# Optimization experiments

Hardware: AMD Instinct MI355X
Metric: run time of the kernel (lower is better)

The kernel has to match this reference:

```python
import jax, jax.numpy as jnp
import numpy as np

N, H, F = 131072, 256, 4096
MIN_FRAG = 3
LN_EPS = 1e-5
NORM_EPS = 1e-12
CONSISTENCY_FACTOR = 0.03
INTERMOLECULAR_WEIGHT = 0.2
SCALING_FACTOR = 0.05  # initial_strength at epoch 0 (progressive schedule, eval mode)


def _normalize(x):
    # torch F.normalize(p=2, dim=1): x / max(||x||, eps)
    n = jnp.linalg.norm(x, axis=-1, keepdims=True)
    return x / jnp.maximum(n, NORM_EPS)


def _frag_consistency(feat, frag_ids, valid):
    # size-weighted sum of per-fragment mean deviations == mean deviation over valid atoms
    m = valid.astype(feat.dtype)[:, None]
    seg_sum = jax.ops.segment_sum(feat * m, frag_ids, num_segments=F)
    seg_cnt = jax.ops.segment_sum(m, frag_ids, num_segments=F)
    means = seg_sum / jnp.maximum(seg_cnt, 1.0)  # scatter-mean over valid atoms
    sim = jnp.sum(_normalize(feat) * _normalize(means)[frag_ids], axis=-1)  # [N]
    dev = (1.0 - sim) * valid.astype(feat.dtype)
    return jnp.sum(dev) / jnp.maximum(jnp.sum(valid.astype(feat.dtype)), 1.0)


def setup_inputs() -> dict:
    key = jax.random.key(0)
    ks = jax.random.split(key, 8)
    return {
        "scalar_short": jax.random.normal(ks[0], (N, H), jnp.float32),
        "scalar_long": jax.random.normal(ks[1], (N, H), jnp.float32),
        "vector_short": jax.random.normal(ks[2], (N, 3, H), jnp.float32),
        "vector_long": jax.random.normal(ks[3], (N, 3, H), jnp.float32),
        "fragment_ids": jax.random.randint(ks[4], (N,), 0, F, dtype=jnp.int32),
        "ln_gamma": jnp.ones((H,), jnp.float32),
        "ln_beta": jnp.zeros((H,), jnp.float32),
        "W1": jax.random.normal(ks[5], (H, H), jnp.float32) / np.sqrt(H),
        "b1": jnp.zeros((H,), jnp.float32),
        "Wv": jax.random.normal(ks[6], (H, H), jnp.float32) / np.sqrt(H),
    }


def reference(scalar_short, scalar_long, vector_short, vector_long, fragment_ids,
              ln_gamma, ln_beta, W1, b1, Wv):
    # valid_mask: atoms belonging to fragments of size >= MIN_FRAG
    sizes = jax.ops.segment_sum(jnp.ones((N,), jnp.float32), fragment_ids, num_segments=F)
    valid = sizes[fragment_ids] >= MIN_FRAG  # [N] bool

    # scalar_projector: LayerNorm -> Linear -> SiLU (dropout identity at eval)
    mu = jnp.mean(scalar_short, axis=-1, keepdims=True)
    var = jnp.var(scalar_short, axis=-1, keepdims=True)
    xh = (scalar_short - mu) / jnp.sqrt(var + LN_EPS) * ln_gamma + ln_beta
    scalar_features = jax.nn.silu(xh @ W1.T + b1)  # [N, H]

    intra = _frag_consistency(scalar_features, fragment_ids, valid)

    # vector branch: per-atom magnitude = mean over 3 spatial comps of ||.||_2 over hidden
    vec_mag = jnp.mean(jnp.linalg.norm(vector_short, axis=2), axis=1, keepdims=True)  # [N,1]
    # Linear(bias=False) on mag.expand(-1,H) then [:, :1] == silu(mag * sum(Wv[0,:]))
    w0 = jnp.sum(Wv[0])
    vector_features = jax.nn.silu(vec_mag * w0)  # [N,1]
    vec_loss = _frag_consistency(vector_features, fragment_ids, valid)

    # interfragment differentiation over ALL atoms (no valid mask)
    cnt = jax.ops.segment_sum(jnp.ones((N, 1), jnp.float32), fragment_ids, num_segments=F)
    sfrag = jax.ops.segment_sum(scalar_features, fragment_ids, num_segments=F) / jnp.maximum(cnt, 1.0)
    vfrag = jax.ops.segment_sum(vec_mag, fragment_ids, num_segments=F) / jnp.maximum(cnt, 1.0)
    combined = _normalize(jnp.concatenate([sfrag, vfrag], axis=1))  # [F, H+1]
    sim = combined @ combined.T  # [F, F]
    off_sum = jnp.sum(sim) - jnp.trace(sim)
    inter = off_sum / (F * F - F + 1e-6)

    total = intra + vec_loss + INTERMOLECULAR_WEIGHT * inter
    return CONSISTENCY_FACTOR * total * SCALING_FACTOR
```

## Files before the change

kernel.cpp:

```cpp
#include <hip/hip_runtime.h>
#include <hip/hip_bf16.h>
#include <stdint.h>

#define NA 131072
#define HD 256
#define NF 4096
#define MINFRAG 3
#define LN_EPS 1e-5f
#define NEPS 1e-12f

#define OFF_CNT    0ull
#define OFF_VSUM   16384ull
#define OFF_VFSUM  32768ull
#define OFF_NVSUM  49152ull
#define OFF_FILL   65536ull
#define OFF_DBL    81920ull
#define OFF_SSUM   86016ull
#define OFF_NSUM   4280320ull
#define ZERO_BYTES 8474624ull
#define OFF_OFFS   8474624ull
#define OFF_SVEC   8491008ull
#define OFF_C0     8492032ull
#define OFF_W0     8493056ull
#define OFF_GBF    8493568ull
#define OFF_ORDER  8624640ull

#define IDX_TRACE 257
#define IDX_DEVS  258
#define IDX_DEVV  259
#define IDX_VCNT  260

typedef __attribute__((ext_vector_type(8))) short short8;
typedef __attribute__((ext_vector_type(4))) float f32x4;
union F4S8 { float4 f; short8 s; };
union BFU { __hip_bfloat16 b; unsigned short u; };

__device__ __forceinline__ unsigned short f2b(float x) {
    BFU t; t.b = __float2bfloat16(x); return t.u;
}
__device__ __forceinline__ float b2f(unsigned short u) {
    return __uint_as_float(((uint32_t)u) << 16);
}
__device__ __forceinline__ float silu_f(float x) { return x / (1.f + expf(-x)); }

__global__ __launch_bounds__(256) void k_prep(
    const float* __restrict__ W1, const float* __restrict__ gamma,
    const float* __restrict__ beta, const float* __restrict__ b1,
    const float* __restrict__ Wv,
    unsigned short* __restrict__ Gbf, float* __restrict__ svec,
    float* __restrict__ c0, float* __restrict__ w0) {
    __shared__ float red[8];
    int o = blockIdx.x;
    int t = threadIdx.x;
    if (o < HD) {
        float w = W1[(size_t)o * HD + t];
        unsigned short gb = f2b(w * gamma[t]);
        Gbf[(size_t)o * HD + t] = gb;
        float sp = b2f(gb);
        float cp = w * beta[t];
#pragma unroll
        for (int m = 32; m; m >>= 1) { sp += __shfl_xor(sp, m, 64); cp += __shfl_xor(cp, m, 64); }
        int wv = t >> 6;
        if ((t & 63) == 0) { red[wv] = sp; red[4 + wv] = cp; }
        __syncthreads();
        if (t == 0) {
            svec[o] = red[0] + red[1] + red[2] + red[3];
            c0[o]   = red[4] + red[5] + red[6] + red[7] + b1[o];
        }
    } else {
        float v = Wv[t];
#pragma unroll
        for (int m = 32; m; m >>= 1) v += __shfl_xor(v, m, 64);
        int wv = t >> 6;
        if ((t & 63) == 0) red[wv] = v;
        __syncthreads();
        if (t == 0) w0[0] = red[0] + red[1] + red[2] + red[3];
    }
}

__global__ __launch_bounds__(256) void k_stats(
    const float* __restrict__ vs, const int* __restrict__ fid,
    const float* __restrict__ w0p,
    int* __restrict__ cnt, float* __restrict__ vsum,
    float* __restrict__ vfsum, float* __restrict__ nvsum) {
    int gwave = (blockIdx.x * blockDim.x + threadIdx.x) >> 6;
    int lane = threadIdx.x & 63;
    int nw = (gridDim.x * blockDim.x) >> 6;
    float w0 = w0p[0];
    for (int i = gwave; i < NA; i += nw) {
        const float* base = vs + (size_t)i * 3 * HD;
        float4 v0 = ((const float4*)(base))[lane];
        float4 v1 = ((const float4*)(base + HD))[lane];
        float4 v2 = ((const float4*)(base + 2 * HD))[lane];
        float q0 = v0.x * v0.x + v0.y * v0.y + v0.z * v0.z + v0.w * v0.w;
        float q1 = v1.x * v1.x + v1.y * v1.y + v1.z * v1.z + v1.w * v1.w;
        float q2 = v2.x * v2.x + v2.y * v2.y + v2.z * v2.z + v2.w * v2.w;
#pragma unroll
        for (int m = 32; m; m >>= 1) {
            q0 += __shfl_xor(q0, m, 64);
            q1 += __shfl_xor(q1, m, 64);
            q2 += __shfl_xor(q2, m, 64);
        }
        if (lane == 0) {
            float vm = (sqrtf(q0) + sqrtf(q1) + sqrtf(q2)) * (1.f / 3.f);
            float vf = silu_f(vm * w0);
            float nv = vf / fmaxf(fabsf(vf), NEPS);
            int f = fid[i];
            atomicAdd(&cnt[f], 1);
            atomicAdd(&vsum[f], vm);
            atomicAdd(&vfsum[f], vf);
            atomicAdd(&nvsum[f], nv);
        }
    }
}

__global__ __launch_bounds__(256) void k_scan(const int* __restrict__ cnt,
                                              int* __restrict__ offs) {
    __shared__ int wsum[4];
    int t = threadIdx.x;
    int base = t * 16;
    int c[16];
    int tot = 0;
#pragma unroll
    for (int j = 0; j < 16; ++j) { c[j] = cnt[base + j]; tot += c[j]; }
    int lane = t & 63, w = t >> 6;
    int v = tot;
#pragma unroll
    for (int d = 1; d < 64; d <<= 1) {
        int o = __shfl_up(v, d, 64);
        if (lane >= d) v += o;
    }
    if (lane == 63) wsum[w] = v;
    __syncthreads();
    int wbase = 0;
    for (int i = 0; i < w; ++i) wbase += wsum[i];
    int run = wbase + v - tot;
#pragma unroll
    for (int j = 0; j < 16; ++j) { offs[base + j] = run; run += c[j]; }
}

__global__ __launch_bounds__(256) void k_scatter(
    const int* __restrict__ fid, const int* __restrict__ offs,
    int* __restrict__ fill, int* __restrict__ order) {
    int i = blockIdx.x * blockDim.x + threadIdx.x;
    if (i < NA) {
        int f = fid[i];
        int p = atomicAdd(&fill[f], 1);
        order[offs[f] + p] = i;
    }
}

__global__ __launch_bounds__(256) void k_gemm(
    const float* __restrict__ A, const unsigned short* __restrict__ Gbf,
    const float* __restrict__ svec, const float* __restrict__ c0,
    const int* __restrict__ order, const int* __restrict__ fid,
    const int* __restrict__ offs, const int* __restrict__ cnt,
    float* __restrict__ ssum, float* __restrict__ nsum) {
    __shared__ float4 As16[64 * 8];
    __shared__ float4 Bs16[256 * 8];
    __shared__ float muS[64], rsS[64], rnS[64];
    __shared__ float sqL[64][4];
    __shared__ int fragS[64];

    int tid = threadIdx.x;
    int lane = tid & 63, wid = tid >> 6;
    int r0 = blockIdx.x * 64;
    int rowT = tid >> 4;
    int c4 = tid & 15;

    if (tid < 64) {
        int gi = order[r0 + tid];
        muS[tid] = __int_as_float(gi);
        fragS[tid] = fid[gi];
    }
    __syncthreads();
    int rid[4];
#pragma unroll
    for (int p = 0; p < 4; ++p) rid[p] = __float_as_int(muS[16 * p + rowT]);
    __syncthreads();

    f32x4 acc[4][4] = {};
    float s1p[4] = {0, 0, 0, 0}, s2p[4] = {0, 0, 0, 0};

    for (int k0 = 0; k0 < HD; k0 += 64) {
#pragma unroll
        for (int p = 0; p < 4; ++p) {
            int row = 16 * p + rowT;
            float4 v = *(const float4*)(A + (size_t)rid[p] * HD + k0 + c4 * 4);
            s1p[p] += v.x + v.y + v.z + v.w;
            s2p[p] += v.x * v.x + v.y * v.y + v.z * v.z + v.w * v.w;
            ushort4 pk;
            pk.x = f2b(v.x); pk.y = f2b(v.y); pk.z = f2b(v.z); pk.w = f2b(v.w);
            int slot = row * 8 + ((c4 >> 1) ^ (row & 7));
            ((ushort4*)&As16[slot])[c4 & 1] = pk;
        }
#pragma unroll
        for (int p = 0; p < 8; ++p) {
            int u = p * 256 + tid;
            int n = u >> 3, cc = u & 7;
            float4 g = *(const float4*)(Gbf + (size_t)n * HD + k0 + cc * 8);
            Bs16[n * 8 + (cc ^ (n & 7))] = g;
        }
        __syncthreads();
#pragma unroll
        for (int kk = 0; kk < 2; ++kk) {
            int uo = kk * 4 + (lane >> 4);
            short8 a[4], b[4];
#pragma unroll
            for (int mi = 0; mi < 4; ++mi) {
                int r = mi * 16 + (lane & 15);
                F4S8 t_; t_.f = As16[r * 8 + (uo ^ (r & 7))];
                a[mi] = t_.s;
            }
#pragma unroll
            for (int ni = 0; ni < 4; ++ni) {
                int n = wid * 64 + ni * 16 + (lane & 15);
                F4S8 t_; t_.f = Bs16[n * 8 + (uo ^ (n & 7))];
                b[ni] = t_.s;
            }
#pragma unroll
            for (int mi = 0; mi < 4; ++mi)
#pragma unroll
                for (int ni = 0; ni < 4; ++ni)
                    acc[mi][ni] = __builtin_amdgcn_mfma_f32_16x16x32_bf16(
                        a[mi], b[ni], acc[mi][ni], 0, 0, 0);
        }
        __syncthreads();
    }
#pragma unroll
    for (int p = 0; p < 4; ++p) {
        float s1 = s1p[p], s2 = s2p[p];
#pragma unroll
        for (int m = 1; m < 16; m <<= 1) {
            s1 += __shfl_xor(s1, m, 64);
            s2 += __shfl_xor(s2, m, 64);
        }
        if (c4 == 0) {
            int row = 16 * p + rowT;
            float mu_ = s1 * (1.f / HD);
            float var = s2 * (1.f / HD) - mu_ * mu_;
            muS[row] = mu_;
            rsS[row] = rsqrtf(var + LN_EPS);
        }
    }
    __syncthreads();
    float sv[4], cv[4];
#pragma unroll
    for (int ni = 0; ni < 4; ++ni) {
        int c = wid * 64 + ni * 16 + (lane & 15);
        sv[ni] = svec[c];
        cv[ni] = c0[c];
    }
    unsigned short* featS = (unsigned short*)Bs16;
    float sq[4][4];
#pragma unroll
    for (int mi = 0; mi < 4; ++mi)
#pragma unroll
        for (int q = 0; q < 4; ++q) {
            int rl = mi * 16 + (lane >> 4) * 4 + q;
            float mu_ = muS[rl], rs_ = rsS[rl];
            float sqa = 0.f;
#pragma unroll
            for (int ni = 0; ni < 4; ++ni) {
                int c = wid * 64 + ni * 16 + (lane & 15);
                float pre = rs_ * (acc[mi][ni][q] - mu_ * sv[ni]) + cv[ni];
                unsigned short us = f2b(silu_f(pre));
                featS[rl * 256 + (c ^ ((rl & 7) << 2))] = us;
                float fr = b2f(us);
                sqa += fr * fr;
            }
            sq[mi][q] = sqa;
        }
#pragma unroll
    for (int mi = 0; mi < 4; ++mi)
#pragma unroll
        for (int q = 0; q < 4; ++q) {
            float s_ = sq[mi][q];
            s_ += __shfl_xor(s_, 1, 64);
            s_ += __shfl_xor(s_, 2, 64);
            s_ += __shfl_xor(s_, 4, 64);
            s_ += __shfl_xor(s_, 8, 64);
            if ((lane & 15) == 0) sqL[mi * 16 + (lane >> 4) * 4 + q][wid] = s_;
        }
    __syncthreads();
    if (tid < 64) {
        float t = sqL[tid][0] + sqL[tid][1] + sqL[tid][2] + sqL[tid][3];
        rnS[tid] = 1.f / fmaxf(sqrtf(t), NEPS);
    }
    __syncthreads();
    int cc = wid * 64 + lane;
    float sAcc = 0.f, nAcc = 0.f;
    int curF = fragS[0];
    for (int row = 0; row < 64; ++row) {
        int f = fragS[row];
        if (f != curF) {
            int gs = offs[curF], n = cnt[curF];
            if (gs >= r0 && gs + n <= r0 + 64) {
                ssum[(size_t)curF * HD + cc] = sAcc;
                nsum[(size_t)curF * HD + cc] = nAcc;
            } else {
                atomicAdd(&ssum[(size_t)curF * HD + cc], sAcc);
                atomicAdd(&nsum[(size_t)curF * HD + cc], nAcc);
            }
            sAcc = 0.f; nAcc = 0.f; curF = f;
        }
        float v = b2f(featS[row * 256 + (cc ^ ((row & 7) << 2))]);
        sAcc += v;
        nAcc = fmaf(v, rnS[row], nAcc);
    }
    {
        int gs = offs[curF], n = cnt[curF];
        if (gs >= r0 && gs + n <= r0 + 64) {
            ssum[(size_t)curF * HD + cc] = sAcc;
            nsum[(size_t)curF * HD + cc] = nAcc;
        } else {
            atomicAdd(&ssum[(size_t)curF * HD + cc], sAcc);
            atomicAdd(&nsum[(size_t)curF * HD + cc], nAcc);
        }
    }
}

__global__ __launch_bounds__(256) void k_frag(
    const float* __restrict__ ssum, const float* __restrict__ nsum,
    const int* __restrict__ cnt, const float* __restrict__ vsum,
    const float* __restrict__ vfsum, const float* __restrict__ nvsum,
    double* __restrict__ dbl) {
    int gwave = (blockIdx.x * blockDim.x + threadIdx.x) >> 6;
    int lane = threadIdx.x & 63;
    int nw = (gridDim.x * blockDim.x) >> 6;

    double la0 = 0, la1 = 0, la2 = 0, la3 = 0;
    double lv = 0, ltr = 0, lvc = 0, ldS = 0, ldV = 0;

    for (int f = gwave; f < NF; f += nw) {
        float4 s = ((const float4*)(ssum + (size_t)f * HD))[lane];
        float4 nn = ((const float4*)(nsum + (size_t)f * HD))[lane];
        int c = cnt[f];
        float ssq = s.x * s.x + s.y * s.y + s.z * s.z + s.w * s.w;
        float dsn = nn.x * s.x + nn.y * s.y + nn.z * s.z + nn.w * s.w;
#pragma unroll
        for (int m = 32; m; m >>= 1) {
            ssq += __shfl_xor(ssq, m, 64);
            dsn += __shfl_xor(dsn, m, 64);
        }
        float inv_all = 1.f / fmaxf((float)c, 1.f);
        float m0 = s.x * inv_all, m1 = s.y * inv_all, m2 = s.z * inv_all, m3 = s.w * inv_all;
        float ssq_mean = ssq * inv_all * inv_all;
        float vfr = vsum[f] * inv_all;
        float nrm2 = ssq_mean + vfr * vfr;
        float inv = 1.f / fmaxf(sqrtf(nrm2), NEPS);
        la0 += (double)(m0 * inv);
        la1 += (double)(m1 * inv);
        la2 += (double)(m2 * inv);
        la3 += (double)(m3 * inv);
        if (lane == 0) {
            lv += (double)(vfr * inv);
            ltr += (double)(nrm2 * inv * inv);
            if (c >= MINFRAG) {
                lvc += (double)c;
                float denom = fmaxf(sqrtf(ssq), NEPS);
                ldS += (double)c - (double)(dsn / denom);
                float vfm = vfsum[f] * inv_all;
                float vsgn = vfm / fmaxf(fabsf(vfm), NEPS);
                ldV += (double)c - (double)(vsgn * nvsum[f]);
            }
        }
    }
    atomicAdd(&dbl[4 * lane + 0], la0);
    atomicAdd(&dbl[4 * lane + 1], la1);
    atomicAdd(&dbl[4 * lane + 2], la2);
    atomicAdd(&dbl[4 * lane + 3], la3);
    if (lane == 0) {
        atomicAdd(&dbl[256], lv);
        atomicAdd(&dbl[IDX_TRACE], ltr);
        atomicAdd(&dbl[IDX_VCNT], lvc);
        atomicAdd(&dbl[IDX_DEVS], ldS);
        atomicAdd(&dbl[IDX_DEVV], ldV);
    }
}

__global__ __launch_bounds__(64) void k_final(const double* __restrict__ dbl,
                                              float* __restrict__ out) {
    if (threadIdx.x == 0 && blockIdx.x == 0) {
        double s2 = 0;
        for (int d = 0; d < 257; ++d) s2 += dbl[d] * dbl[d];
        double off = s2 - dbl[IDX_TRACE];
        double inter = off / ((double)NF * NF - NF + 1e-6);
        double vc = fmax(dbl[IDX_VCNT], 1.0);
        double total = dbl[IDX_DEVS] / vc + dbl[IDX_DEVV] / vc + 0.2 * inter;
        out[0] = (float)(0.03 * 0.05 * total);
    }
}

extern "C" void kernel_launch(void* const* d_in, const int* in_sizes, int n_in,
                              void* d_out, int out_size, void* d_ws, size_t ws_size,
                              hipStream_t stream) {
    const float* scalar_short = (const float*)d_in[0];
    const float* vector_short = (const float*)d_in[2];
    const int* fragment_ids = (const int*)d_in[4];
    const float* ln_gamma = (const float*)d_in[5];
    const float* ln_beta = (const float*)d_in[6];
    const float* W1 = (const float*)d_in[7];
    const float* b1 = (const float*)d_in[8];
    const float* Wv = (const float*)d_in[9];
    float* out = (float*)d_out;

    char* ws = (char*)d_ws;
    int* cnt = (int*)(ws + OFF_CNT);
    float* vsum = (float*)(ws + OFF_VSUM);
    float* vfsum = (float*)(ws + OFF_VFSUM);
    float* nvsum = (float*)(ws + OFF_NVSUM);
    int* fill = (int*)(ws + OFF_FILL);
    double* dbl = (double*)(ws + OFF_DBL);
    float* ssum = (float*)(ws + OFF_SSUM);
    float* nsum = (float*)(ws + OFF_NSUM);
    int* offs = (int*)(ws + OFF_OFFS);
    float* svec = (float*)(ws + OFF_SVEC);
    float* c0 = (float*)(ws + OFF_C0);
    float* w0 = (float*)(ws + OFF_W0);
    unsigned short* Gbf = (unsigned short*)(ws + OFF_GBF);
    int* order = (int*)(ws + OFF_ORDER);

    hipMemsetAsync(ws, 0, ZERO_BYTES, stream);
    k_prep<<<HD + 1, 256, 0, stream>>>(W1, ln_gamma, ln_beta, b1, Wv, Gbf, svec, c0, w0);
    k_stats<<<2048, 256, 0, stream>>>(vector_short, fragment_ids, w0, cnt, vsum, vfsum, nvsum);
    k_scan<<<1, 256, 0, stream>>>(cnt, offs);
    k_scatter<<<NA / 256, 256, 0, stream>>>(fragment_ids, offs, fill, order);
    k_gemm<<<NA / 64, 256, 0, stream>>>(scalar_short, Gbf, svec, c0, order,
                                        fragment_ids, offs, cnt, ssum, nsum);
    k_frag<<<64, 256, 0, stream>>>(ssum, nsum, cnt, vsum, vfsum, nvsum, dbl);
    k_final<<<1, 64, 0, stream>>>(dbl, out);
}
```

Baseline: 252.7 us.

## Fuse prep, fragment counting and buffer zeroing; regroup vector-stats waves

Weight preparation, per-fragment atom counting and zeroing of the large ssum/nsum buffers now happen in one 512-block kernel, so the memset only covers the small header. The count no longer waits on the heavy vector-stats pass, which moves after the scatter. Vector stats now handle four atoms per wave with 16 lanes each, which shortens the shuffle reductions and uses a faster SiLU intrinsic. The GEMM drops one barrier by giving row ids their own shared array, and k_frag launches with more blocks. Correctness depends on k_frag handling the larger grid and on zbuf exactly covering the ssum/nsum range.

```diff
diff --git a/kernel.cpp b/kernel.cpp
--- a/kernel.cpp
+++ b/kernel.cpp
@@ -15,9 +15,9 @@
 #define OFF_NVSUM  49152ull
 #define OFF_FILL   65536ull
 #define OFF_DBL    81920ull
+#define ZERO_HEAD  84224ull
 #define OFF_SSUM   86016ull
 #define OFF_NSUM   4280320ull
-#define ZERO_BYTES 8474624ull
 #define OFF_OFFS   8474624ull
 #define OFF_SVEC   8491008ull
 #define OFF_C0     8492032ull
@@ -41,77 +41,55 @@
 __device__ __forceinline__ float b2f(unsigned short u) {
     return __uint_as_float(((uint32_t)u) << 16);
 }
-__device__ __forceinline__ float silu_f(float x) { return x / (1.f + expf(-x)); }
-
-__global__ __launch_bounds__(256) void k_prep(
-    const float* __restrict__ W1, const float* __restrict__ gamma,
-    const float* __restrict__ beta, const float* __restrict__ b1,
-    const float* __restrict__ Wv,
-    unsigned short* __restrict__ Gbf, float* __restrict__ svec,
-    float* __restrict__ c0, float* __restrict__ w0) {
+__device__ __forceinline__ float silu_f(float x) {
+    return x * __builtin_amdgcn_rcpf(1.f + __expf(-x));
+}
+
+__global__ __launch_bounds__(256) void k_pre(
+    const int* __restrict__ fid, const float* __restrict__ W1,
+    const float* __restrict__ gamma, const float* __restrict__ beta,
+    const float* __restrict__ b1, const float* __restrict__ Wv,
+    int* __restrict__ cnt, unsigned short* __restrict__ Gbf,
+    float* __restrict__ svec, float* __restrict__ c0, float* __restrict__ w0,
+    float4* __restrict__ zbuf) {
+    int b = blockIdx.x;
+    int t = threadIdx.x;
     __shared__ float red[8];
-    int o = blockIdx.x;
-    int t = threadIdx.x;
-    if (o < HD) {
-        float w = W1[(size_t)o * HD + t];
-        unsigned short gb = f2b(w * gamma[t]);
-        Gbf[(size_t)o * HD + t] = gb;
-        float sp = b2f(gb);
-        float cp = w * beta[t];
-#pragma unroll
-        for (int m = 32; m; m >>= 1) { sp += __shfl_xor(sp, m, 64); cp += __shfl_xor(cp, m, 64); }
-        int wv = t >> 6;
-        if ((t & 63) == 0) { red[wv] = sp; red[4 + wv] = cp; }
-        __syncthreads();
-        if (t == 0) {
-            svec[o] = red[0] + red[1] + red[2] + red[3];
-            c0[o]   = red[4] + red[5] + red[6] + red[7] + b1[o];
-        }
-    } else {
-        float v = Wv[t];
-#pragma unroll
-        for (int m = 32; m; m >>= 1) v += __shfl_xor(v, m, 64);
-        int wv = t >> 6;
-        if ((t & 63) == 0) red[wv] = v;
-        __syncthreads();
-        if (t == 0) w0[0] = red[0] + red[1] + red[2] + red[3];
-    }
-}
-
-__global__ __launch_bounds__(256) void k_stats(
-    const float* __restrict__ vs, const int* __restrict__ fid,
-    const float* __restrict__ w0p,
-    int* __restrict__ cnt, float* __restrict__ vsum,
-    float* __restrict__ vfsum, float* __restrict__ nvsum) {
-    int gwave = (blockIdx.x * blockDim.x + threadIdx.x) >> 6;
-    int lane = threadIdx.x & 63;
-    int nw = (gridDim.x * blockDim.x) >> 6;
-    float w0 = w0p[0];
-    for (int i = gwave; i < NA; i += nw) {
-        const float* base = vs + (size_t)i * 3 * HD;
-        float4 v0 = ((const float4*)(base))[lane];
-        float4 v1 = ((const float4*)(base + HD))[lane];
-        float4 v2 = ((const float4*)(base + 2 * HD))[lane];
-        float q0 = v0.x * v0.x + v0.y * v0.y + v0.z * v0.z + v0.w * v0.w;
-        float q1 = v1.x * v1.x + v1.y * v1.y + v1.z * v1.z + v1.w * v1.w;
-        float q2 = v2.x * v2.x + v2.y * v2.y + v2.z * v2.z + v2.w * v2.w;
-#pragma unroll
-        for (int m = 32; m; m >>= 1) {
-            q0 += __shfl_xor(q0, m, 64);
-            q1 += __shfl_xor(q1, m, 64);
-            q2 += __shfl_xor(q2, m, 64);
-        }
-        if (lane == 0) {
-            float vm = (sqrtf(q0) + sqrtf(q1) + sqrtf(q2)) * (1.f / 3.f);
-            float vf = silu_f(vm * w0);
-            float nv = vf / fmaxf(fabsf(vf), NEPS);
-            int f = fid[i];
-            atomicAdd(&cnt[f], 1);
-            atomicAdd(&vsum[f], vm);
-            atomicAdd(&vfsum[f], vf);
-            atomicAdd(&nvsum[f], nv);
-        }
-    }
+    if (b < 257) {
+        if (b < HD) {
+            int o = b;
+            float w = W1[(size_t)o * HD + t];
+            unsigned short gb = f2b(w * gamma[t]);
+            Gbf[(size_t)o * HD + t] = gb;
+            float sp = b2f(gb);
+            float cp = w * beta[t];
+#pragma unroll
+            for (int m = 32; m; m >>= 1) {
+                sp += __shfl_xor(sp, m, 64);
+                cp += __shfl_xor(cp, m, 64);
+            }
+            int wv = t >> 6;
+            if ((t & 63) == 0) { red[wv] = sp; red[4 + wv] = cp; }
+            __syncthreads();
+            if (t == 0) {
+                svec[o] = red[0] + red[1] + red[2] + red[3];
+                c0[o]   = red[4] + red[5] + red[6] + red[7] + b1[o];
+            }
+        } else {
+            float v = Wv[t];
+#pragma unroll
+            for (int m = 32; m; m >>= 1) v += __shfl_xor(v, m, 64);
+            int wv = t >> 6;
+            if ((t & 63) == 0) red[wv] = v;
+            __syncthreads();
+            if (t == 0) w0[0] = red[0] + red[1] + red[2] + red[3];
+        }
+    }
+    float4 zv = {0.f, 0.f, 0.f, 0.f};
+#pragma unroll
+    for (int j = 0; j < 4; ++j) zbuf[(size_t)b * 1024 + j * 256 + t] = zv;
+    int i = b * 256 + t;
+    atomicAdd(&cnt[fid[i]], 1);
 }
 
 __global__ __launch_bounds__(256) void k_scan(const int* __restrict__ cnt,
@@ -147,6 +125,47 @@
         int f = fid[i];
         int p = atomicAdd(&fill[f], 1);
         order[offs[f] + p] = i;
+    }
+}
+
+__global__ __launch_bounds__(256) void k_stats(
+    const float* __restrict__ vs, const int* __restrict__ fid,
+    const float* __restrict__ w0p,
+    float* __restrict__ vsum, float* __restrict__ vfsum,
+    float* __restrict__ nvsum) {
+    int gwave = (blockIdx.x * blockDim.x + threadIdx.x) >> 6;
+    int lane = threadIdx.x & 63;
+    int nw = (gridDim.x * blockDim.x) >> 6;
+    int g = lane >> 4, sl = lane & 15;
+    float w0 = w0p[0];
+    for (int i0 = gwave * 4; i0 < NA; i0 += nw * 4) {
+        int i = i0 + g;
+        const float* vb = vs + (size_t)i * 3 * HD;
+        float q0 = 0.f, q1 = 0.f, q2 = 0.f;
+#pragma unroll
+        for (int j = 0; j < 4; ++j) {
+            float4 a = ((const float4*)(vb))[sl * 4 + j];
+            float4 b = ((const float4*)(vb + HD))[sl * 4 + j];
+            float4 c = ((const float4*)(vb + 2 * HD))[sl * 4 + j];
+            q0 += a.x * a.x + a.y * a.y + a.z * a.z + a.w * a.w;
+            q1 += b.x * b.x + b.y * b.y + b.z * b.z + b.w * b.w;
+            q2 += c.x * c.x + c.y * c.y + c.z * c.z + c.w * c.w;
+        }
+#pragma unroll
+        for (int m = 1; m < 16; m <<= 1) {
+            q0 += __shfl_xor(q0, m, 64);
+            q1 += __shfl_xor(q1, m, 64);
+            q2 += __shfl_xor(q2, m, 64);
+        }
+        if (sl == 0) {
+            float vm = (sqrtf(q0) + sqrtf(q1) + sqrtf(q2)) * (1.f / 3.f);
+            float vf = silu_f(vm * w0);
+            float nv = vf / fmaxf(fabsf(vf), NEPS);
+            int f = fid[i];
+            atomicAdd(&vsum[f], vm);
+            atomicAdd(&vfsum[f], vf);
+            atomicAdd(&nvsum[f], nv);
+        }
     }
 }
 
@@ -160,7 +179,7 @@
     __shared__ float4 Bs16[256 * 8];
     __shared__ float muS[64], rsS[64], rnS[64];
     __shared__ float sqL[64][4];
-    __shared__ int fragS[64];
+    __shared__ int ridS[64], fragS[64];
 
     int tid = threadIdx.x;
     int lane = tid & 63, wid = tid >> 6;
@@ -170,19 +189,19 @@
 
     if (tid < 64) {
         int gi = order[r0 + tid];
-        muS[tid] = __int_as_float(gi);
+        ridS[tid] = gi;
         fragS[tid] = fid[gi];
     }
     __syncthreads();
     int rid[4];
 #pragma unroll
-    for (int p = 0; p < 4; ++p) rid[p] = __float_as_int(muS[16 * p + rowT]);
-    __syncthreads();
+    for (int p = 0; p < 4; ++p) rid[p] = ridS[16 * p + rowT];
 
     f32x4 acc[4][4] = {};
     float s1p[4] = {0, 0, 0, 0}, s2p[4] = {0, 0, 0, 0};
 
-    for (int k0 = 0; k0 < HD; k0 += 64) {
+    for (int kc = 0; kc < 4; ++kc) {
+        int k0 = kc * 64;
 #pragma unroll
         for (int p = 0; p < 4; ++p) {
             int row = 16 * p + rowT;
@@ -205,7 +224,7 @@
 #pragma unroll
         for (int kk = 0; kk < 2; ++kk) {
             int uo = kk * 4 + (lane >> 4);
-            short8 a[4], b[4];
+            short8 a[4], bfr[4];
 #pragma unroll
             for (int mi = 0; mi < 4; ++mi) {
                 int r = mi * 16 + (lane & 15);
@@ -216,14 +235,14 @@
             for (int ni = 0; ni < 4; ++ni) {
                 int n = wid * 64 + ni * 16 + (lane & 15);
                 F4S8 t_; t_.f = Bs16[n * 8 + (uo ^ (n & 7))];
-                b[ni] = t_.s;
+                bfr[ni] = t_.s;
             }
 #pragma unroll
             for (int mi = 0; mi < 4; ++mi)
 #pragma unroll
                 for (int ni = 0; ni < 4; ++ni)
                     acc[mi][ni] = __builtin_amdgcn_mfma_f32_16x16x32_bf16(
-                        a[mi], b[ni], acc[mi][ni], 0, 0, 0);
+                        a[mi], bfr[ni], acc[mi][ni], 0, 0, 0);
         }
         __syncthreads();
     }
@@ -421,13 +440,14 @@
     unsigned short* Gbf = (unsigned short*)(ws + OFF_GBF);
     int* order = (int*)(ws + OFF_ORDER);
 
-    hipMemsetAsync(ws, 0, ZERO_BYTES, stream);
-    k_prep<<<HD + 1, 256, 0, stream>>>(W1, ln_gamma, ln_beta, b1, Wv, Gbf, svec, c0, w0);
-    k_stats<<<2048, 256, 0, stream>>>(vector_short, fragment_ids, w0, cnt, vsum, vfsum, nvsum);
+    hipMemsetAsync(ws, 0, ZERO_HEAD, stream);
+    k_pre<<<512, 256, 0, stream>>>(fragment_ids, W1, ln_gamma, ln_beta, b1, Wv,
+                                   cnt, Gbf, svec, c0, w0, (float4*)(ws + OFF_SSUM));
     k_scan<<<1, 256, 0, stream>>>(cnt, offs);
     k_scatter<<<NA / 256, 256, 0, stream>>>(fragment_ids, offs, fill, order);
+    k_stats<<<2048, 256, 0, stream>>>(vector_short, fragment_ids, w0, vsum, vfsum, nvsum);
     k_gemm<<<NA / 64, 256, 0, stream>>>(scalar_short, Gbf, svec, c0, order,
                                         fragment_ids, offs, cnt, ssum, nsum);
-    k_frag<<<64, 256, 0, stream>>>(ssum, nsum, cnt, vsum, vfsum, nvsum, dbl);
+    k_frag<<<512, 256, 0, stream>>>(ssum, nsum, cnt, vsum, vfsum, nvsum, dbl);
     k_final<<<1, 64, 0, stream>>>(dbl, out);
 }
```

Measured after the change: 393.7 us. 1.56x slower.
